# Performance work log

Hardware: AMD Instinct MI355X
Metric: run time of the kernel (lower is better)

The kernel has to match this reference:

```python
import jax, jax.numpy as jnp
import numpy as np

N = 100000
E = 3200000
D_IN = 128
D_OUT = 128
ALPHA = 0.2  # LeakyReLU negative slope
LN_EPS = 1e-5


def setup_inputs() -> dict:
    key = jax.random.key(0)
    k1, k2, k3, k4, k5 = jax.random.split(key, 5)
    x = jax.random.normal(k1, (N, D_IN), dtype=jnp.float32)
    edge = jax.random.randint(k2, (2, E), 0, N, dtype=jnp.int64)
    # Linear params (kaiming-normal-ish init)
    W = jax.random.normal(k3, (D_OUT, D_IN), dtype=jnp.float32) * np.sqrt(2.0 / D_IN)
    b = jnp.zeros((D_OUT,), dtype=jnp.float32)
    # attention vector a: (2*out,)
    a = jax.random.normal(k4, (2 * D_OUT,), dtype=jnp.float32) * np.sqrt(2.0 / (2 * D_OUT))
    ln_w = jnp.ones((D_OUT,), dtype=jnp.float32)
    ln_b = jnp.zeros((D_OUT,), dtype=jnp.float32)
    return {"x": x, "W": W, "b": b, "a": a, "ln_w": ln_w, "ln_b": ln_b, "edge": edge}


def reference(x, W, b, a, ln_w, ln_b, edge):
    n = x.shape[0]
    d_out = W.shape[0]
    h = x @ W.T + b  # [N, D_OUT]
    src, dst = edge[0], edge[1]
    # a.mm(cat(h[src], h[dst]).T) == h[src] @ a1 + h[dst] @ a2
    a1, a2 = a[:d_out], a[d_out:]
    node_s1 = h @ a1  # [N]
    node_s2 = h @ a2  # [N]
    z = node_s1[src] + node_s2[dst]  # [E]
    edge_e = jnp.exp(-jax.nn.leaky_relu(z, ALPHA))  # [E]
    # sparse spmm: h_prime[i] = sum_{e: src=i} edge_e[e] * h[dst[e]]
    msgs = edge_e[:, None] * h[dst]  # [E, D_OUT]
    h_prime = jax.ops.segment_sum(msgs, src, num_segments=n)  # [N, D_OUT]
    # LayerNorm over last dim
    mu = jnp.mean(h_prime, axis=-1, keepdims=True)
    var = jnp.mean(jnp.square(h_prime - mu), axis=-1, keepdims=True)
    h_norm = (h_prime - mu) * jax.lax.rsqrt(var + LN_EPS) * ln_w + ln_b
    return jax.nn.elu(h_norm)
```

## Files before the change

### kernel.cpp

```cpp
#include <hip/hip_runtime.h>
#include <math.h>

#define D 128
#define GAT_ALPHA 0.2f
#define LN_EPS 1e-5f
#define BSHIFT 5
#define BKT 32
#define NBMAX 3200
#define CAPB 1280
#define ECHUNK 16384
#define XPITCH 136

typedef __attribute__((ext_vector_type(8))) short short8;
typedef __attribute__((ext_vector_type(4))) float floatx4;

__device__ __forceinline__ unsigned short f2bf(float f) {
    unsigned u = __float_as_uint(f);
    unsigned r = (u + 0x7fffu + ((u >> 16) & 1u)) >> 16;
    return (unsigned short)r;
}
__device__ __forceinline__ float bfl(unsigned u) { return __uint_as_float(u << 16); }
__device__ __forceinline__ float bfh(unsigned u) { return __uint_as_float(u & 0xffff0000u); }

__global__ __launch_bounds__(256) void prep_bfrag(const float* __restrict__ W,
                                                  unsigned short* __restrict__ Bfrag)
{
    for (int idx = threadIdx.x; idx < 2048; idx += 256) {
        int lane = idx & 63, ntkt = idx >> 6;
        int nt = ntkt >> 2, kt = ntkt & 3;
        int l16 = lane & 15, quad = lane >> 4;
        const float* wp = W + (size_t)(nt * 16 + l16) * D + kt * 32 + quad * 8;
        unsigned short* op = Bfrag + (size_t)idx * 8;
#pragma unroll
        for (int j = 0; j < 8; ++j) op[j] = f2bf(wp[j]);
    }
}

union SmemU {
    struct { unsigned short Bf[16384]; unsigned short xs[128 * XPITCH]; } g;
    struct { int cnt[NBMAX]; int basex[NBMAX]; int cnt2x[NBMAX]; } p;
};

__global__ __launch_bounds__(512) void gemm_partition(
        const float* __restrict__ x, const unsigned short* __restrict__ Bfrag_g,
        const float* __restrict__ b, const float* __restrict__ a,
        const int* __restrict__ src, const int* __restrict__ dst,
        int* __restrict__ gcnt, int* __restrict__ pairs,
        unsigned short* __restrict__ h16, float* __restrict__ s1,
        float* __restrict__ s2, int n, int nE, int nb, int npart)
{
    __shared__ SmemU sm;
    const int tid = threadIdx.x;

    if (blockIdx.x < npart) {
        int* cnt = sm.p.cnt; int* basex = sm.p.basex; int* cnt2x = sm.p.cnt2x;
        for (int i = tid; i < nb; i += 512) { cnt[i] = 0; cnt2x[i] = 0; }
        __syncthreads();
        int e0 = blockIdx.x * ECHUNK;
        int e1 = e0 + ECHUNK; if (e1 > nE) e1 = nE;
        for (int e = e0 + tid; e < e1; e += 512)
            atomicAdd(&cnt[src[e] >> BSHIFT], 1);
        __syncthreads();
        for (int i = tid; i < nb; i += 512)
            basex[i] = cnt[i] ? atomicAdd(&gcnt[i], cnt[i]) : 0;
        __syncthreads();
        for (int e = e0 + tid; e < e1; e += 512) {
            int s = src[e];
            int bb = s >> BSHIFT;
            int l = basex[bb] + atomicAdd(&cnt2x[bb], 1);
            if (l < CAPB) pairs[(size_t)bb * CAPB + l] = ((s & (BKT - 1)) << 24) | dst[e];
        }
        return;
    }

    unsigned short* Bf = sm.g.Bf;
    unsigned short* xs = sm.g.xs;
    {
        const uint2* sp = (const uint2*)Bfrag_g;
        uint2* dp = (uint2*)Bf;
        for (int i = tid; i < 4096; i += 512) dp[i] = sp[i];
    }
    const int lane = tid & 63, wave = tid >> 6;
    const int l16 = lane & 15, quad = lane >> 4;
    const int row0 = (blockIdx.x - npart) * 128;

    for (int i = tid; i < 4096; i += 512) {
        int row = i >> 5, c4 = i & 31;
        float4 v = make_float4(0.f, 0.f, 0.f, 0.f);
        if (row0 + row < n) v = *(const float4*)(x + (size_t)(row0 + row) * D + c4 * 4);
        ushort4 o;
        o.x = f2bf(v.x); o.y = f2bf(v.y); o.z = f2bf(v.z); o.w = f2bf(v.w);
        *(ushort4*)&xs[row * XPITCH + c4 * 4] = o;
    }

    float bcol[8], a1c[8], a2c[8];
#pragma unroll
    for (int nt = 0; nt < 8; ++nt) {
        int c = nt * 16 + l16;
        bcol[nt] = b[c]; a1c[nt] = a[c]; a2c[nt] = a[D + c];
    }
    __syncthreads();

    floatx4 acc[8];
#pragma unroll
    for (int nt = 0; nt < 8; ++nt) acc[nt] = (floatx4){0.f, 0.f, 0.f, 0.f};

#pragma unroll
    for (int kt = 0; kt < 4; ++kt) {
        short8 af = *(const short8*)&xs[(wave * 16 + l16) * XPITCH + kt * 32 + quad * 8];
#pragma unroll
        for (int nt = 0; nt < 8; ++nt) {
            short8 bf = *(const short8*)&Bf[(size_t)((nt * 4 + kt) * 64 + lane) * 8];
            acc[nt] = __builtin_amdgcn_mfma_f32_16x16x32_bf16(af, bf, acc[nt], 0, 0, 0);
        }
    }

    float hv[4][8];
#pragma unroll
    for (int r = 0; r < 4; ++r) {
        float p1 = 0.f, p2 = 0.f;
#pragma unroll
        for (int nt = 0; nt < 8; ++nt) {
            float v = acc[nt][r] + bcol[nt];
            hv[r][nt] = v;
            p1 = fmaf(v, a1c[nt], p1);
            p2 = fmaf(v, a2c[nt], p2);
        }
#pragma unroll
        for (int off = 8; off > 0; off >>= 1) {
            p1 += __shfl_xor(p1, off);
            p2 += __shfl_xor(p2, off);
        }
        int crow = row0 + wave * 16 + quad * 4 + r;
        if (crow < n && l16 == 0) { s1[crow] = p1; s2[crow] = p2; }
    }

    __syncthreads();
#pragma unroll
    for (int r = 0; r < 4; ++r)
#pragma unroll
        for (int nt = 0; nt < 8; ++nt)
            xs[(wave * 16 + quad * 4 + r) * XPITCH + nt * 16 + l16] = f2bf(hv[r][nt]);
    __syncthreads();

    for (int i = tid; i < 2048; i += 512) {
        int row = i >> 4, c = i & 15;
        if (row0 + row < n)
            *(uint4*)(h16 + (size_t)(row0 + row) * D + c * 8) =
                *(const uint4*)&xs[row * XPITCH + c * 8];
    }
}

__global__ __launch_bounds__(128, 6) void sort_aggregate(const int* __restrict__ pairs,
                                                         const int* __restrict__ gcnt,
                                                         const float* __restrict__ s1,
                                                         const float* __restrict__ s2,
                                                         const unsigned short* __restrict__ h16,
                                                         const float* __restrict__ ln_w,
                                                         const float* __restrict__ ln_b,
                                                         float* __restrict__ out, int n)
{
    __shared__ int2 csr2[CAPB];
    __shared__ int cnt[BKT], cnt2[BKT], excl[BKT + 1];
    __shared__ float sA[BKT];

    const int bkt = blockIdx.x, tid = threadIdx.x;
    const size_t base = (size_t)bkt * CAPB;
    int m = gcnt[bkt]; if (m > CAPB) m = CAPB;

    if (tid < BKT) {
        cnt[tid] = 0; cnt2[tid] = 0;
        int node = bkt * BKT + tid;
        sA[tid] = (node < n) ? s1[node] : 0.f;
    }
    __syncthreads();

    for (int e = tid; e < m; e += 128)
        atomicAdd(&cnt[((unsigned)pairs[base + e]) >> 24], 1);
    __syncthreads();

    if (tid < 32) {
        int v = cnt[tid], incl = v;
#pragma unroll
        for (int off = 1; off < 32; off <<= 1) {
            int t = __shfl_up(incl, off);
            if (tid >= off) incl += t;
        }
        excl[tid] = incl - v;
        if (tid == 31) excl[32] = incl;
    }
    __syncthreads();

    for (int e = tid; e < m; e += 128) {
        int w = pairs[base + e];
        int sl = ((unsigned)w) >> 24;
        int d = w & 0xFFFFFF;
        float z = sA[sl] + s2[d];
        float lz = z > 0.f ? z : GAT_ALPHA * z;
        float ee = __expf(-lz);
        int pos = excl[sl] + atomicAdd(&cnt2[sl], 1);
        csr2[pos] = make_int2(d, __float_as_int(ee));
    }
    __syncthreads();

    const int lane = tid & 63, wv = tid >> 6;
    const int q = lane >> 4, l16 = lane & 15;

    for (int i = 0; i < 16; ++i) {
        int nl = wv * 16 + i;
        int node = bkt * BKT + nl;
        if (node >= n) break;
        int e0 = excl[nl], e1 = excl[nl + 1];

        float acc[8];
#pragma unroll
        for (int j = 0; j < 8; ++j) acc[j] = 0.f;

        int e = e0 + q;
        for (; e + 12 < e1; e += 16) {
            int2 pa = csr2[e];
            int2 pb = csr2[e + 4];
            int2 pc = csr2[e + 8];
            int2 pd = csr2[e + 12];
            uint4 ua = *(const uint4*)(h16 + (size_t)pa.x * D + l16 * 8);
            uint4 ub = *(const uint4*)(h16 + (size_t)pb.x * D + l16 * 8);
            uint4 uc = *(const uint4*)(h16 + (size_t)pc.x * D + l16 * 8);
            uint4 ud = *(const uint4*)(h16 + (size_t)pd.x * D + l16 * 8);
            float ea = __int_as_float(pa.y);
            float eb = __int_as_float(pb.y);
            float ec = __int_as_float(pc.y);
            float ed = __int_as_float(pd.y);
            acc[0] = fmaf(ea, bfl(ua.x), acc[0]);
            acc[1] = fmaf(ea, bfh(ua.x), acc[1]);
            acc[2] = fmaf(ea, bfl(ua.y), acc[2]);
            acc[3] = fmaf(ea, bfh(ua.y), acc[3]);
            acc[4] = fmaf(ea, bfl(ua.z), acc[4]);
            acc[5] = fmaf(ea, bfh(ua.z), acc[5]);
            acc[6] = fmaf(ea, bfl(ua.w), acc[6]);
            acc[7] = fmaf(ea, bfh(ua.w), acc[7]);
            acc[0] = fmaf(eb, bfl(ub.x), acc[0]);
            acc[1] = fmaf(eb, bfh(ub.x), acc[1]);
            acc[2] = fmaf(eb, bfl(ub.y), acc[2]);
            acc[3] = fmaf(eb, bfh(ub.y), acc[3]);
            acc[4] = fmaf(eb, bfl(ub.z), acc[4]);
            acc[5] = fmaf(eb, bfh(ub.z), acc[5]);
            acc[6] = fmaf(eb, bfl(ub.w), acc[6]);
            acc[7] = fmaf(eb, bfh(ub.w), acc[7]);
            acc[0] = fmaf(ec, bfl(uc.x), acc[0]);
            acc[1] = fmaf(ec, bfh(uc.x), acc[1]);
            acc[2] = fmaf(ec, bfl(uc.y), acc[2]);
            acc[3] = fmaf(ec, bfh(uc.y), acc[3]);
            acc[4] = fmaf(ec, bfl(uc.z), acc[4]);
            acc[5] = fmaf(ec, bfh(uc.z), acc[5]);
            acc[6] = fmaf(ec, bfl(uc.w), acc[6]);
            acc[7] = fmaf(ec, bfh(uc.w), acc[7]);
            acc[0] = fmaf(ed, bfl(ud.x), acc[0]);
            acc[1] = fmaf(ed, bfh(ud.x), acc[1]);
            acc[2] = fmaf(ed, bfl(ud.y), acc[2]);
            acc[3] = fmaf(ed, bfh(ud.y), acc[3]);
            acc[4] = fmaf(ed, bfl(ud.z), acc[4]);
            acc[5] = fmaf(ed, bfh(ud.z), acc[5]);
            acc[6] = fmaf(ed, bfl(ud.w), acc[6]);
            acc[7] = fmaf(ed, bfh(ud.w), acc[7]);
        }
        for (; e < e1; e += 4) {
            int2 p = csr2[e];
            float ee = __int_as_float(p.y);
            uint4 u = *(const uint4*)(h16 + (size_t)p.x * D + l16 * 8);
            acc[0] = fmaf(ee, bfl(u.x), acc[0]);
            acc[1] = fmaf(ee, bfh(u.x), acc[1]);
            acc[2] = fmaf(ee, bfl(u.y), acc[2]);
            acc[3] = fmaf(ee, bfh(u.y), acc[3]);
            acc[4] = fmaf(ee, bfl(u.z), acc[4]);
            acc[5] = fmaf(ee, bfh(u.z), acc[5]);
            acc[6] = fmaf(ee, bfl(u.w), acc[6]);
            acc[7] = fmaf(ee, bfh(u.w), acc[7]);
        }
#pragma unroll
        for (int j = 0; j < 8; ++j) acc[j] += __shfl_down(acc[j], 32);
#pragma unroll
        for (int j = 0; j < 8; ++j) acc[j] += __shfl_down(acc[j], 16);

        float sum = 0.f, sq = 0.f;
#pragma unroll
        for (int j = 0; j < 8; ++j) { sum += acc[j]; sq += acc[j] * acc[j]; }
#pragma unroll
        for (int off = 8; off > 0; off >>= 1) {
            sum += __shfl_xor(sum, off);
            sq  += __shfl_xor(sq, off);
        }

        if (q == 0) {
            float mu   = sum * (1.0f / 128.0f);
            float var  = sq * (1.0f / 128.0f) - mu * mu;
            float rstd = rsqrtf(var + LN_EPS);

            float4 w0 = *(const float4*)(ln_w + l16 * 8);
            float4 w1 = *(const float4*)(ln_w + l16 * 8 + 4);
            float4 b0 = *(const float4*)(ln_b + l16 * 8);
            float4 b1 = *(const float4*)(ln_b + l16 * 8 + 4);
            float y[8];
            y[0] = (acc[0] - mu) * rstd * w0.x + b0.x;
            y[1] = (acc[1] - mu) * rstd * w0.y + b0.y;
            y[2] = (acc[2] - mu) * rstd * w0.z + b0.z;
            y[3] = (acc[3] - mu) * rstd * w0.w + b0.w;
            y[4] = (acc[4] - mu) * rstd * w1.x + b1.x;
            y[5] = (acc[5] - mu) * rstd * w1.y + b1.y;
            y[6] = (acc[6] - mu) * rstd * w1.z + b1.z;
            y[7] = (acc[7] - mu) * rstd * w1.w + b1.w;
#pragma unroll
            for (int j = 0; j < 8; ++j) y[j] = y[j] > 0.f ? y[j] : expm1f(y[j]);
            float* op = out + (size_t)node * D + l16 * 8;
            *(float4*)op       = make_float4(y[0], y[1], y[2], y[3]);
            *(float4*)(op + 4) = make_float4(y[4], y[5], y[6], y[7]);
        }
    }
}

extern "C" void kernel_launch(void* const* d_in, const int* in_sizes, int n_in,
                              void* d_out, int out_size, void* d_ws, size_t ws_size,
                              hipStream_t stream)
{
    const float* x    = (const float*)d_in[0];
    const float* W    = (const float*)d_in[1];
    const float* b    = (const float*)d_in[2];
    const float* a    = (const float*)d_in[3];
    const float* ln_w = (const float*)d_in[4];
    const float* ln_b = (const float*)d_in[5];
    const int*   edge = (const int*)d_in[6];

    const int n  = in_sizes[0] / D;
    const int nE = in_sizes[6] / 2;
    const int* src = edge;
    const int* dst = edge + nE;
    const int nb = (n + BKT - 1) >> BSHIFT;
    const int npart = (nE + ECHUNK - 1) / ECHUNK;
    const int ngemm = (n + 127) / 128;

    float* out = (float*)d_out;

    unsigned short* h16 = (unsigned short*)d_ws;
    float* s1   = (float*)(h16 + (size_t)n * D);
    float* s2   = s1 + n;
    unsigned short* Bfrag = (unsigned short*)(s2 + n);
    int* pairs  = (int*)(Bfrag + 16384);
    int* gcnt   = pairs + (size_t)nb * CAPB;

    hipMemsetAsync(gcnt, 0, (size_t)nb * sizeof(int), stream);

    prep_bfrag    <<<1, 256, 0, stream>>>(W, Bfrag);
    gemm_partition<<<npart + ngemm, 512, 0, stream>>>(x, Bfrag, b, a, src, dst,
                                                      gcnt, pairs, h16, s1, s2,
                                                      n, nE, nb, npart);
    sort_aggregate<<<nb, 128, 0, stream>>>(pairs, gcnt, s1, s2, h16, ln_w, ln_b, out, n);
}
```

Baseline: 328.3 us.

## Fold W bf16 prep into GEMM blocks; give each node its own 16-lane group

Removes the separate single-block prep_bfrag launch. Each GEMM block now converts W to bf16 fragments directly into shared memory, trading one small kernel launch for redundant W reads and conversions in every block. The aggregation loop is also restructured: each 16-lane group handles one node and walks all of its edges serially, instead of a whole wave splitting a node's edges across four quads. This drops the cross-quad shuffle reduction and processes 4 nodes per wave concurrently, but per-lane gather chains get longer and load balance now depends on node degree.

```diff
diff --git a/kernel.cpp b/kernel.cpp
--- a/kernel.cpp
+++ b/kernel.cpp
@@ -22,27 +22,13 @@
 __device__ __forceinline__ float bfl(unsigned u) { return __uint_as_float(u << 16); }
 __device__ __forceinline__ float bfh(unsigned u) { return __uint_as_float(u & 0xffff0000u); }
 
-__global__ __launch_bounds__(256) void prep_bfrag(const float* __restrict__ W,
-                                                  unsigned short* __restrict__ Bfrag)
-{
-    for (int idx = threadIdx.x; idx < 2048; idx += 256) {
-        int lane = idx & 63, ntkt = idx >> 6;
-        int nt = ntkt >> 2, kt = ntkt & 3;
-        int l16 = lane & 15, quad = lane >> 4;
-        const float* wp = W + (size_t)(nt * 16 + l16) * D + kt * 32 + quad * 8;
-        unsigned short* op = Bfrag + (size_t)idx * 8;
-#pragma unroll
-        for (int j = 0; j < 8; ++j) op[j] = f2bf(wp[j]);
-    }
-}
-
 union SmemU {
     struct { unsigned short Bf[16384]; unsigned short xs[128 * XPITCH]; } g;
     struct { int cnt[NBMAX]; int basex[NBMAX]; int cnt2x[NBMAX]; } p;
 };
 
 __global__ __launch_bounds__(512) void gemm_partition(
-        const float* __restrict__ x, const unsigned short* __restrict__ Bfrag_g,
+        const float* __restrict__ x, const float* __restrict__ W,
         const float* __restrict__ b, const float* __restrict__ a,
         const int* __restrict__ src, const int* __restrict__ dst,
         int* __restrict__ gcnt, int* __restrict__ pairs,
@@ -75,11 +61,21 @@
 
     unsigned short* Bf = sm.g.Bf;
     unsigned short* xs = sm.g.xs;
-    {
-        const uint2* sp = (const uint2*)Bfrag_g;
-        uint2* dp = (uint2*)Bf;
-        for (int i = tid; i < 4096; i += 512) dp[i] = sp[i];
-    }
+
+    for (int idx = tid; idx < 2048; idx += 512) {
+        int lane = idx & 63, ntkt = idx >> 6;
+        int nt = ntkt >> 2, kt = ntkt & 3;
+        int bl16 = lane & 15, bquad = lane >> 4;
+        const float* wp = W + (size_t)(nt * 16 + bl16) * D + kt * 32 + bquad * 8;
+        float4 w0 = *(const float4*)wp;
+        float4 w1 = *(const float4*)(wp + 4);
+        ushort4 o0, o1;
+        o0.x = f2bf(w0.x); o0.y = f2bf(w0.y); o0.z = f2bf(w0.z); o0.w = f2bf(w0.w);
+        o1.x = f2bf(w1.x); o1.y = f2bf(w1.y); o1.z = f2bf(w1.z); o1.w = f2bf(w1.w);
+        *(ushort4*)&Bf[idx * 8]     = o0;
+        *(ushort4*)&Bf[idx * 8 + 4] = o1;
+    }
+
     const int lane = tid & 63, wave = tid >> 6;
     const int l16 = lane & 15, quad = lane >> 4;
     const int row0 = (blockIdx.x - npart) * 128;
@@ -203,25 +199,27 @@
     }
     __syncthreads();
 
-    const int lane = tid & 63, wv = tid >> 6;
-    const int q = lane >> 4, l16 = lane & 15;
-
-    for (int i = 0; i < 16; ++i) {
-        int nl = wv * 16 + i;
+    const int gq = tid >> 4;
+    const int l16 = tid & 15;
+
+#pragma unroll 1
+    for (int i = 0; i < BKT / 8; ++i) {
+        int nl = i * 8 + gq;
         int node = bkt * BKT + nl;
-        if (node >= n) break;
-        int e0 = excl[nl], e1 = excl[nl + 1];
+        bool alive = node < n;
+        int e0 = alive ? excl[nl] : 0;
+        int e1 = alive ? excl[nl + 1] : 0;
 
         float acc[8];
 #pragma unroll
         for (int j = 0; j < 8; ++j) acc[j] = 0.f;
 
-        int e = e0 + q;
-        for (; e + 12 < e1; e += 16) {
+        int e = e0;
+        for (; e + 3 < e1; e += 4) {
             int2 pa = csr2[e];
-            int2 pb = csr2[e + 4];
-            int2 pc = csr2[e + 8];
-            int2 pd = csr2[e + 12];
+            int2 pb = csr2[e + 1];
+            int2 pc = csr2[e + 2];
+            int2 pd = csr2[e + 3];
             uint4 ua = *(const uint4*)(h16 + (size_t)pa.x * D + l16 * 8);
             uint4 ub = *(const uint4*)(h16 + (size_t)pb.x * D + l16 * 8);
             uint4 uc = *(const uint4*)(h16 + (size_t)pc.x * D + l16 * 8);
@@ -263,7 +261,7 @@
             acc[6] = fmaf(ed, bfl(ud.w), acc[6]);
             acc[7] = fmaf(ed, bfh(ud.w), acc[7]);
         }
-        for (; e < e1; e += 4) {
+        for (; e < e1; ++e) {
             int2 p = csr2[e];
             float ee = __int_as_float(p.y);
             uint4 u = *(const uint4*)(h16 + (size_t)p.x * D + l16 * 8);
@@ -276,10 +274,6 @@
             acc[6] = fmaf(ee, bfl(u.w), acc[6]);
             acc[7] = fmaf(ee, bfh(u.w), acc[7]);
         }
-#pragma unroll
-        for (int j = 0; j < 8; ++j) acc[j] += __shfl_down(acc[j], 32);
-#pragma unroll
-        for (int j = 0; j < 8; ++j) acc[j] += __shfl_down(acc[j], 16);
 
         float sum = 0.f, sq = 0.f;
 #pragma unroll
@@ -290,7 +284,7 @@
             sq  += __shfl_xor(sq, off);
         }
 
-        if (q == 0) {
+        if (alive) {
             float mu   = sum * (1.0f / 128.0f);
             float var  = sq * (1.0f / 128.0f) - mu * mu;
             float rstd = rsqrtf(var + LN_EPS);
@@ -342,14 +336,12 @@
     unsigned short* h16 = (unsigned short*)d_ws;
     float* s1   = (float*)(h16 + (size_t)n * D);
     float* s2   = s1 + n;
-    unsigned short* Bfrag = (unsigned short*)(s2 + n);
-    int* pairs  = (int*)(Bfrag + 16384);
+    int* pairs  = (int*)(s2 + n);
     int* gcnt   = pairs + (size_t)nb * CAPB;
 
     hipMemsetAsync(gcnt, 0, (size_t)nb * sizeof(int), stream);
 
-    prep_bfrag    <<<1, 256, 0, stream>>>(W, Bfrag);
-    gemm_partition<<<npart + ngemm, 512, 0, stream>>>(x, Bfrag, b, a, src, dst,
+    gemm_partition<<<npart + ngemm, 512, 0, stream>>>(x, W, b, a, src, dst,
                                                       gcnt, pairs, h16, s1, s2,
                                                       n, nE, nb, npart);
     sort_aggregate<<<nb, 128, 0, stream>>>(pairs, gcnt, s1, s2, h16, ln_w, ln_b, out, n);
```

Result: no change. 322.6 us (-1.7%).
